# Kernel optimization log

Measured on AMD Instinct MI355X. Metric: run time of the kernel, lower is better.

## Reference

```python
import jax, jax.numpy as jnp
import numpy as np

INPUT_SIZE = 256
NUM_LABELS = 50
L = NUM_LABELS + 1  # internal label count incl. pad label (index L-1)
B, T = 64, 256


def setup_inputs() -> dict:
    key = jax.random.key(0)
    k = jax.random.split(key, 8)
    inp = {
        "input": jax.random.normal(k[0], (B, T, INPUT_SIZE), dtype=jnp.float32),
        "mask": jnp.ones((B, T), dtype=jnp.float32),
        "target": jax.random.randint(k[1], (B, T), 0, NUM_LABELS),
        # state_nn: Linear(input_size, L)
        "state_W": jax.random.normal(k[2], (INPUT_SIZE, L), dtype=jnp.float32) * 0.05,
        "state_b": jnp.zeros((L,), dtype=jnp.float32),
        # trans_nn: Linear(input_size, L*L) (bigram=True)
        "trans_W": jax.random.normal(k[3], (INPUT_SIZE, L * L), dtype=jnp.float32) * 0.05,
        "trans_b": jnp.zeros((L * L,), dtype=jnp.float32),
    }
    return inp


def _energy(x, mask, state_W, state_b, trans_W, trans_b):
    # out_s: [B,T,L]  (unary scores), out_t: [B,T,L,L] (bigram transitions)
    out_s = jnp.einsum("bti,il->btl", x, state_W) + state_b
    out_t = (jnp.einsum("bti,io->bto", x, trans_W) + trans_b).reshape(
        x.shape[0], x.shape[1], L, L
    )
    energy = out_t + out_s[:, :, None, :]  # [B,T,L,L]
    return energy * mask[:, :, None, None]


def reference(input, mask, target, state_W, state_b, trans_W, trans_b):
    """ChainCRF.loss: -log p(target | input) per batch element, shape [B]."""
    energy = _energy(input, mask, state_W, state_b, trans_W, trans_b)
    e_t = jnp.transpose(energy, (1, 0, 2, 3))  # [T,B,L,L]
    tgt_t = target.T                            # [T,B]
    msk_t = mask.T                              # [T,B]
    bidx = jnp.arange(input.shape[0])

    # t = 0: start from pad label (index L-1)
    partition0 = e_t[0][:, L - 1, :]                       # [B,L]
    tgt0 = e_t[0][bidx, L - 1, tgt_t[0]]                   # [B]

    def step(carry, xs):
        part, tgt_e, prev = carry
        curr, tgt, m = xs  # curr [B,L,L], tgt [B], m [B]
        part_new = jax.nn.logsumexp(curr + part[:, :, None], axis=1)
        part = part + (part_new - part) * m[:, None]
        tgt_e = tgt_e + curr[bidx, prev, tgt]
        return (part, tgt_e, tgt), None

    (part, tgt_e, _), _ = jax.lax.scan(
        step, (partition0, tgt0, tgt_t[0]), (e_t[1:], tgt_t[1:], msk_t[1:])
    )
    return jax.nn.logsumexp(part, axis=1) - tgt_e
```

## Files before the change

### kernel.cpp

```cpp
#include <hip/hip_runtime.h>
#include <hip/hip_bf16.h>

#define B_    64
#define T_    256
#define K_    256
#define L_    51
#define LL_   2601
#define RS_   64
#define NG_   3328
#define PST_  4096
#define MT_   128
#define NT_   128

typedef __bf16 bf16x8 __attribute__((ext_vector_type(8)));
typedef float  f32x4  __attribute__((ext_vector_type(4)));
typedef unsigned int u32x4 __attribute__((ext_vector_type(4)));
typedef u32x4 __attribute__((may_alias)) u32x4_a;
typedef unsigned long long ull;
typedef ull __attribute__((may_alias)) ull_a;
typedef unsigned short ushort_a __attribute__((may_alias));

static __device__ __forceinline__ bf16x8 as_bf16x8(u32x4 u) {
    return __builtin_bit_cast(bf16x8, u);
}
static __device__ __forceinline__ unsigned short bf16bits(float x) {
    return __builtin_bit_cast(unsigned short, __float2bfloat16(x));
}
static __device__ __forceinline__ ull pack4(f32x4 a) {
    return (ull)bf16bits(a[0]) | ((ull)bf16bits(a[1]) << 16) |
           ((ull)bf16bits(a[2]) << 32) | ((ull)bf16bits(a[3]) << 48);
}
static __device__ __forceinline__ void gld_lds16(const void* g, void* l) {
    __builtin_amdgcn_global_load_lds(
        (const __attribute__((address_space(1))) unsigned int*)g,
        (__attribute__((address_space(3))) unsigned int*)l, 16, 0, 0);
}

#define DPP_STEP(v, OP, CTRL)                                                   \
    {                                                                           \
        int _x = __builtin_bit_cast(int, v);                                    \
        float _o = __builtin_bit_cast(                                          \
            float, __builtin_amdgcn_update_dpp(_x, _x, CTRL, 0xF, 0xF, true));  \
        v = OP(v, _o);                                                          \
    }
static __device__ __forceinline__ float addf(float a, float b) { return a + b; }

__global__ __launch_bounds__(256) void prep_all(
    const float* __restrict__ trans_W, const float* __restrict__ trans_b,
    const float* __restrict__ state_W, const float* __restrict__ state_b,
    const float* __restrict__ x,
    __hip_bfloat16* __restrict__ Wt, float* __restrict__ bias,
    __hip_bfloat16* __restrict__ xb, __hip_bfloat16* __restrict__ P, int Tc)
{
    __shared__ __align__(16) __hip_bfloat16 Wl[52 * 258];
    const int blk = blockIdx.x, tid = threadIdx.x;

    if (blk < 64) {
        const int i = blk;
        if (i < L_) {
            const int jp = tid & 63, kk = tid >> 6;
            if (jp < 52) {
                for (int k = kk; k < K_; k += 4) {
                    float v = 0.f;
                    if (jp < L_) v = trans_W[(size_t)k * LL_ + i * L_ + jp] +
                                     state_W[k * L_ + jp];
                    Wl[jp * 258 + k] = __float2bfloat16(v);
                }
            }
            __syncthreads();
            for (int idx = tid; idx < 52 * 32; idx += 256) {
                const int j = idx >> 5, c = idx & 31;
                const unsigned int* row = (const unsigned int*)&Wl[j * 258];
                u32x4 v;
                v[0] = row[c * 4 + 0]; v[1] = row[c * 4 + 1];
                v[2] = row[c * 4 + 2]; v[3] = row[c * 4 + 3];
                *(u32x4*)(Wt + (size_t)((j << 6) + i) * K_ + c * 8) = v;
            }
        } else {
            const u32x4 z = {};
            for (int idx = tid; idx < 52 * 32; idx += 256) {
                const int j = idx >> 5, c = idx & 31;
                *(u32x4*)(Wt + (size_t)((j << 6) + i) * K_ + c * 8) = z;
            }
        }
        if (tid < 52) {
            const int j = tid;
            bias[(j << 6) + i] =
                (i < L_ && j < L_) ? trans_b[i * L_ + j] + state_b[j] : 0.f;
        }
    } else if (blk < 64 + 1024) {
        const int n4 = B_ * T_ * K_ / 4;
        const float4* x4 = (const float4*)x;
        ushort4* xb4 = (ushort4*)xb;
        for (int idx = (blk - 64) * 256 + tid; idx < n4; idx += 1024 * 256) {
            float4 v = x4[idx];
            ushort4 o;
            o.x = bf16bits(v.x); o.y = bf16bits(v.y);
            o.z = bf16bits(v.z); o.w = bf16bits(v.w);
            xb4[idx] = o;
        }
    } else {
        const int per = (PST_ - NG_) / 8;
        const int tot = B_ * Tc * per;
        u32x4* P16 = (u32x4*)P;
        const u32x4 z = {};
        for (int idx = (blk - 1088) * 256 + tid; idx < tot; idx += 1024 * 256) {
            const int m = idx / per;
            const int q = idx - m * per;
            P16[(size_t)m * (PST_ / 8) + (NG_ / 8) + q] = z;
        }
    }
}

__global__ __launch_bounds__(256) void gemm_energy(
    const __hip_bfloat16* __restrict__ xb,
    const __hip_bfloat16* __restrict__ Wt,
    const float* __restrict__ bias,
    const float* __restrict__ mask,
    __hip_bfloat16* __restrict__ P,
    int t0, int Tc, int TcShift)
{
    __shared__ __align__(16) __hip_bfloat16 As[MT_ * 64];
    __shared__ __align__(16) __hip_bfloat16 Bs[NT_ * 64];

    const int tid  = threadIdx.x;
    const int lane = tid & 63;
    const int wv   = tid >> 6;
    const int quad = lane >> 4;
    const int l16  = lane & 15;
    const int m0 = blockIdx.y * MT_;
    const int n0 = blockIdx.x * NT_;
    const int mrow0 = (wv >> 1) * 64;
    const int ncol0 = (wv & 1) * 64;

    f32x4 acc[4][4] = {};

    for (int kp = 0; kp < 4; ++kp) {
        if (kp) __syncthreads();
#pragma unroll
        for (int it = 0; it < 4; ++it) {
            const int s = it * 256 + tid;
            const int r = s >> 3;
            const int c = (lane & 7) ^ (r & 7);
            const int ma = m0 + r;
            const int rg = (ma >> TcShift) * T_ + t0 + (ma & (Tc - 1));
            gld_lds16((const char*)xb + (size_t)rg * 512 + kp * 128 + c * 16,
                      (char*)As + it * 4096 + wv * 1024);
            gld_lds16((const char*)Wt + (size_t)(n0 + r) * 512 + kp * 128 + c * 16,
                      (char*)Bs + it * 4096 + wv * 1024);
        }
        asm volatile("s_waitcnt vmcnt(0)" ::: "memory");
        __syncthreads();

        const u32x4_a* Av = (const u32x4_a*)As;
        const u32x4_a* Bv = (const u32x4_a*)Bs;
#pragma unroll
        for (int kk = 0; kk < 2; ++kk) {
            bf16x8 af[4], bfr[4];
#pragma unroll
            for (int f = 0; f < 4; ++f) {
                const int ra = mrow0 + f * 16 + l16;
                af[f]  = as_bf16x8(Av[ra * 8 + ((kk * 4 + quad) ^ (ra & 7))]);
                const int rb = ncol0 + f * 16 + l16;
                bfr[f] = as_bf16x8(Bv[rb * 8 + ((kk * 4 + quad) ^ (rb & 7))]);
            }
#pragma unroll
            for (int mf = 0; mf < 4; ++mf)
#pragma unroll
                for (int nf = 0; nf < 4; ++nf)
                    acc[mf][nf] = __builtin_amdgcn_mfma_f32_16x16x32_bf16(
                        af[mf], bfr[nf], acc[mf][nf], 0, 0, 0);
        }
    }
    __syncthreads();

    char* E = (char*)As;
    const int jcol = (n0 + ncol0) >> 6;
    const bool jok = jcol < L_;
    float bv[4]; bool ok[4]; int ii[4];
#pragma unroll
    for (int nf = 0; nf < 4; ++nf) {
        const int n = n0 + ncol0 + nf * 16 + l16;
        ii[nf]   = nf * 16 + l16;
        ok[nf]   = jok && (ii[nf] < L_);
        bv[nf]   = bias[n];
    }
#pragma unroll
    for (int mf = 0; mf < 4; ++mf) {
#pragma unroll
        for (int r = 0; r < 4; ++r) {
            const int ml = mrow0 + mf * 16 + quad * 4 + r;
            const int m  = m0 + ml;
            const int bb = m >> TcShift;
            const int tl = m & (Tc - 1);
            const int t  = t0 + tl;
            const float mval = mask[bb * T_ + t];
            const bool idm = (mval == 0.f) && (t != 0);
            char* erow = E + ml * 256;
            const int rot = (ml * 8) & 255;
#pragma unroll
            for (int nf = 0; nf < 4; ++nf) {
                float v;
                if (idm) v = (ok[nf] && ii[nf] == jcol) ? 1.f : 0.f;
                else     v = ok[nf] ? __expf((acc[mf][nf][r] + bv[nf]) * mval) : 0.f;
                const int nloc = ncol0 + nf * 16 + l16;
                *(ushort_a*)(erow + ((nloc * 2 + rot) & 255)) = bf16bits(v);
            }
        }
    }
    __syncthreads();

#pragma unroll
    for (int it2 = 0; it2 < 8; ++it2) {
        const int idx = it2 * 256 + tid;
        const int ml = idx >> 4, c = idx & 15;
        const char* erow = E + ml * 256;
        const int rot = (ml * 8) & 255;
        const ull lo = *(const ull_a*)(erow + ((c * 16 + rot) & 255));
        const ull hi = *(const ull_a*)(erow + ((c * 16 + 8 + rot) & 255));
        u32x4 v;
        v[0] = (unsigned int)lo; v[1] = (unsigned int)(lo >> 32);
        v[2] = (unsigned int)hi; v[3] = (unsigned int)(hi >> 32);
        *(u32x4*)(P + (size_t)(m0 + ml) * PST_ + n0 + c * 8) = v;
    }
}

__global__ __launch_bounds__(256) void prod_quad(
    const __hip_bfloat16* __restrict__ P,
    __hip_bfloat16* __restrict__ Q,
    int Tc)
{
    __shared__ u32x4 Sm[4][512];
    __shared__ __align__(16) unsigned short Tb[2][64 * 64];

    unsigned short* W2t = (unsigned short*)&Sm[0][0];
    unsigned short* W4b = (unsigned short*)&Sm[2][0];

    const int tid  = threadIdx.x;
    const int wv   = tid >> 6;
    const int lane = tid & 63;
    const int quad = lane >> 4;
    const int l16  = lane & 15;
    const int bq = blockIdx.x;
    const int Tq = Tc >> 2;
    const int b  = bq / Tq;
    const int tq = bq - b * Tq;
    const __hip_bfloat16* tile0 = P + (size_t)(b * Tc + tq * 4) * PST_;

#pragma unroll
    for (int q = 0; q < 8; ++q) {
        const int idx  = q * 4 + wv;
        const int tile = idx >> 3;
        const int part = idx & 7;
        const int slot = part * 64 + lane;
        const int r    = slot >> 3;
        const int csrc = (slot & 7) ^ (r & 7);
        gld_lds16((const char*)(tile0 + (size_t)tile * PST_) + (r * 8 + csrc) * 16,
                  (char*)&Sm[tile][part * 64]);
    }

    u32x4 idf[2];
    {
        const int e = l16 & 7;
        const unsigned int bits = (e & 1) ? 0x3F800000u : 0x3F80u;
#pragma unroll
        for (int par = 0; par < 2; ++par) {
            u32x4 v = {};
            if (quad == (l16 >> 3) + par * 2) v[e >> 1] = bits;
            idf[par] = v;
        }
    }

    auto twr = [&](unsigned short* buf, int rb, int colb, ull v) {
        *(ull_a*)((char*)buf + rb * 128 + ((colb + 16 * (rb & 7)) & 127)) = v;
    };
    auto trd = [&](const unsigned short* buf, int r, int colb) -> u32x4 {
        return *(const u32x4_a*)((char*)buf + r * 128 + ((colb + 16 * (r & 7)) & 127));
    };
    const int wcol = wv * 32 + quad * 8;

    const int ra = wv * 16 + l16;
    const f32x4 z = {};
    asm volatile("s_waitcnt vmcnt(0)" ::: "memory");
    __syncthreads();

#pragma unroll
    for (int tt = 0; tt < 2; ++tt) {
        const u32x4* S = Sm[tt * 2];
        bf16x8 a0 = as_bf16x8(S[ra * 8 + (quad ^ (ra & 7))]);
        bf16x8 a1 = as_bf16x8(S[ra * 8 + ((4 + quad) ^ (ra & 7))]);
#pragma unroll
        for (int nf = 0; nf < 4; ++nf) {
            f32x4 d = __builtin_amdgcn_mfma_f32_16x16x32_bf16(
                (nf >> 1) ? a1 : a0, as_bf16x8(idf[nf & 1]), z, 0, 0, 0);
            twr(Tb[tt], nf * 16 + l16, wcol, pack4(d));
        }
    }
    __syncthreads();

    {
        bf16x8 a2[2], a3[2];
#pragma unroll
        for (int ks = 0; ks < 2; ++ks) {
            a2[ks] = as_bf16x8(Sm[1][ra * 8 + ((ks * 4 + quad) ^ (ra & 7))]);
            a3[ks] = as_bf16x8(trd(Tb[1], ra, ks * 64 + quad * 16));
        }
        ull w2v[4], w4v[4];
#pragma unroll
        for (int nf = 0; nf < 4; ++nf) {
            const int rb = nf * 16 + l16;
            f32x4 u = z, v = z;
#pragma unroll
            for (int ks = 0; ks < 2; ++ks) {
                bf16x8 bU = as_bf16x8(trd(Tb[0], rb, ks * 64 + quad * 16));
                bf16x8 bV = as_bf16x8(Sm[3][rb * 8 + ((ks * 4 + quad) ^ (rb & 7))]);
                u = __builtin_amdgcn_mfma_f32_16x16x32_bf16(a2[ks], bU, u, 0, 0, 0);
                v = __builtin_amdgcn_mfma_f32_16x16x32_bf16(a3[ks], bV, v, 0, 0, 0);
            }
            w2v[nf] = pack4(u);
            w4v[nf] = pack4(v);
        }
        __syncthreads();
#pragma unroll
        for (int nf = 0; nf < 4; ++nf) {
            twr(W2t, nf * 16 + l16, wcol, w2v[nf]);
            twr(W4b, nf * 16 + l16, wcol, w4v[nf]);
        }
    }
    __syncthreads();

    {
        bf16x8 aw[2];
#pragma unroll
        for (int ks = 0; ks < 2; ++ks)
            aw[ks] = as_bf16x8(trd(W2t, ra, ks * 64 + quad * 16));
        ull mv[4];
#pragma unroll
        for (int nf = 0; nf < 4; ++nf) {
            const int rb = nf * 16 + l16;
            f32x4 d = z;
#pragma unroll
            for (int ks = 0; ks < 2; ++ks) {
                bf16x8 bw = as_bf16x8(trd(W4b, rb, ks * 64 + quad * 16));
                d = __builtin_amdgcn_mfma_f32_16x16x32_bf16(aw[ks], bw, d, 0, 0, 0);
            }
            mv[nf] = pack4(d);
        }
        __syncthreads();
#pragma unroll
        for (int nf = 0; nf < 4; ++nf)
            twr(Tb[0], nf * 16 + l16, wcol, mv[nf]);
    }
    __syncthreads();

    u32x4* qout = (u32x4*)(Q + (size_t)bq * PST_);
#pragma unroll
    for (int c = tid; c < 512; c += 256) {
        const int row = c >> 3;
        const int pos = c & 7;
        qout[row * 8 + pos] = trd(Tb[0], row, pos * 16);
    }
}

__global__ __launch_bounds__(128, 1) void scan_q(
    const __hip_bfloat16* __restrict__ Q,
    const __hip_bfloat16* __restrict__ P,
    const int* __restrict__ target, const float* __restrict__ mask,
    float* __restrict__ p_ws, float* __restrict__ ls_ws,
    float* __restrict__ tgt_ws, float* __restrict__ out,
    int t0q, int Tq, int Tqtot)
{
    __shared__ __align__(16) unsigned short p_arr[64];
    __shared__ float tgt_sh;

    const int b    = blockIdx.x;
    const int tid  = threadIdx.x;
    const int wv   = tid >> 6;
    const int lane = tid & 63;
    const int quad = lane >> 4;
    const int l16  = lane & 15;
    const int t0 = t0q << 2, Tc = Tq << 2;

    float pv[4] = {0.f, 0.f, 0.f, 0.f};
    float logscale = 0.f;

    if (wv == 0) {
        if (t0q == 0) {
            p_arr[lane] = (lane == L_ - 1) ? (unsigned short)0x3F80 : (unsigned short)0;
        } else {
#pragma unroll
            for (int f = 0; f < 4; ++f) pv[f] = p_ws[b * 64 + f * 16 + l16];
            logscale = ls_ws[b];
            p_arr[quad * 16 + l16] = bf16bits(pv[quad]);
        }
        asm volatile("s_waitcnt lgkmcnt(0)" ::: "memory");

        int off[8];
#pragma unroll
        for (int f = 0; f < 4; ++f)
#pragma unroll
            for (int ks = 0; ks < 2; ++ks)
                off[f * 2 + ks] = (f * 16 + l16) * 8 + ks * 4 + quad;

        const u32x4* gp = (const u32x4*)Q + (size_t)b * Tq * (PST_ / 8);
        const u32x4_a* pa = (const u32x4_a*)p_arr;

        u32x4 s0[8], s1[8], s2[8], s3[8];
        auto fetch = [&](u32x4 (&st)[8], int tl) {
            const u32x4* g = gp + (size_t)tl * (PST_ / 8);
#pragma unroll
            for (int q = 0; q < 8; ++q) st[q] = g[off[q]];
        };
        fetch(s0, 0);
        if (1 < Tq) fetch(s1, 1);
        if (2 < Tq) fetch(s2, 2);
        if (3 < Tq) fetch(s3, 3);

        auto step = [&](u32x4 (&st)[8], int tl) {
            bf16x8 a0 = as_bf16x8(pa[quad]);
            bf16x8 a1 = as_bf16x8(pa[4 + quad]);
            const f32x4 z = {};
            f32x4 ae[4], ao[4];
#pragma unroll
            for (int f = 0; f < 4; ++f) {
                ae[f] = __builtin_amdgcn_mfma_f32_16x16x32_bf16(a0, as_bf16x8(st[f * 2 + 0]), z, 0, 0, 0);
                ao[f] = __builtin_amdgcn_mfma_f32_16x16x32_bf16(a1, as_bf16x8(st[f * 2 + 1]), z, 0, 0, 0);
            }
#pragma unroll
            for (int f = 0; f < 4; ++f) pv[f] = ae[f][0] + ao[f][0];

            if (((tl & 1) == 1) || (tl == Tq - 1)) {
                float mx = fmaxf(fmaxf(pv[0], pv[1]), fmaxf(pv[2], pv[3]));
                DPP_STEP(mx, fmaxf, 0xB1);
                DPP_STEP(mx, fmaxf, 0x4E);
                DPP_STEP(mx, fmaxf, 0x124);
                DPP_STEP(mx, fmaxf, 0x128);
                const float inv = 1.f / mx;
                logscale += __logf(mx);
#pragma unroll
                for (int f = 0; f < 4; ++f) pv[f] *= inv;
            }
            p_arr[quad * 16 + l16] = bf16bits(pv[quad]);
            asm volatile("s_waitcnt lgkmcnt(0)" ::: "memory");
        };

        for (int tl = 0; tl < Tq; tl += 4) {
            step(s0, tl);
            if (tl + 4 < Tq) fetch(s0, tl + 4);
            if (tl + 1 < Tq) { step(s1, tl + 1); if (tl + 5 < Tq) fetch(s1, tl + 5); }
            if (tl + 2 < Tq) { step(s2, tl + 2); if (tl + 6 < Tq) fetch(s2, tl + 6); }
            if (tl + 3 < Tq) { step(s3, tl + 3); if (tl + 7 < Tq) fetch(s3, tl + 7); }
        }
    } else {
        float s = 0.f;
        for (int tl = lane; tl < Tc; tl += 64) {
            const int t = t0 + tl;
            const int j = target[b * T_ + t];
            const int i = (t == 0) ? (L_ - 1) : target[b * T_ + t - 1];
            const float m = (t == 0) ? 1.f : mask[b * T_ + t];
            if (m != 0.f) {
                const float pval =
                    __bfloat162float(P[(size_t)(b * Tc + tl) * PST_ + j * RS_ + i]);
                s += __logf(pval);
            }
        }
#pragma unroll
        for (int d = 1; d < 64; d <<= 1) s += __shfl_xor(s, d);
        if (lane == 0) {
            const float tot = (t0 == 0) ? s : tgt_ws[b] + s;
            tgt_ws[b] = tot;
            tgt_sh = tot;
        }
    }
    __syncthreads();

    if (wv == 0) {
        if (t0q + Tq == Tqtot) {
            float s = pv[0] + pv[1] + pv[2] + pv[3];
            DPP_STEP(s, addf, 0xB1);
            DPP_STEP(s, addf, 0x4E);
            DPP_STEP(s, addf, 0x124);
            DPP_STEP(s, addf, 0x128);
            if (lane == 0) out[b] = logscale + __logf(s) - tgt_sh;
        } else {
            if (quad == 0) {
#pragma unroll
                for (int f = 0; f < 4; ++f) p_ws[b * 64 + f * 16 + l16] = pv[f];
            }
            if (lane == 0) ls_ws[b] = logscale;
        }
    }
}

extern "C" void kernel_launch(void* const* d_in, const int* in_sizes, int n_in,
                              void* d_out, int out_size, void* d_ws, size_t ws_size,
                              hipStream_t stream)
{
    (void)in_sizes; (void)n_in; (void)out_size;
    const float* x       = (const float*)d_in[0];
    const float* mask    = (const float*)d_in[1];
    const int*   target  = (const int*)d_in[2];
    const float* state_W = (const float*)d_in[3];
    const float* state_b = (const float*)d_in[4];
    const float* trans_W = (const float*)d_in[5];
    const float* trans_b = (const float*)d_in[6];
    float* out = (float*)d_out;

    char* ws = (char*)d_ws;
    size_t off = 0;
    auto alloc = [&](size_t bytes) -> void* {
        void* p = ws + off;
        off = (off + bytes + 255) & ~(size_t)255;
        return p;
    };

    __hip_bfloat16* Wt   = (__hip_bfloat16*)alloc((size_t)NG_ * K_ * 2);
    float*          bias = (float*)alloc((size_t)NG_ * 4);
    __hip_bfloat16* xb   = (__hip_bfloat16*)alloc((size_t)B_ * T_ * K_ * 2);
    float*          p_ws = (float*)alloc((size_t)B_ * 64 * 4);
    float*          ls   = (float*)alloc((size_t)B_ * 4);
    float*          tgte = (float*)alloc((size_t)B_ * 4);
    const size_t fixed = off;

    int Tc = 256;
    while (Tc > 4 && fixed + (size_t)Tc * B_ * PST_ * 2 * 5 / 4 + 512 > ws_size) Tc >>= 1;
    __hip_bfloat16* P = (__hip_bfloat16*)alloc((size_t)Tc * B_ * PST_ * 2);
    __hip_bfloat16* Q = (__hip_bfloat16*)alloc((size_t)(Tc / 4) * B_ * PST_ * 2);
    int TcShift = 0;
    while ((1 << TcShift) < Tc) ++TcShift;

    prep_all<<<dim3(2112), 256, 0, stream>>>(
        trans_W, trans_b, state_W, state_b, x, Wt, bias, xb, P, Tc);

    for (int t0 = 0; t0 < T_; t0 += Tc) {
        gemm_energy<<<dim3(NG_ / NT_, (B_ * Tc) / MT_), 256, 0, stream>>>(
            xb, Wt, bias, mask, P, t0, Tc, TcShift);
        prod_quad<<<dim3(B_ * (Tc / 4)), 256, 0, stream>>>(P, Q, Tc);
        scan_q<<<dim3(B_), 128, 0, stream>>>(Q, P, target, mask, p_ws, ls, tgte, out,
                                             t0 / 4, Tc / 4, T_ / 4);
    }
}
```

Baseline: 209.6 us.

## Double-buffer GEMM loads, fold bias and log2e into weights, shrink P stride

The GEMM now double-buffers its K-slice loads in LDS, so global-to-LDS copies overlap the MFMA work. Bias goes into the accumulator init and log2(e) is folded into the weights, so the epilogue is a bare exp2 with a fast path when every mask value in the wave is 1. The P buffer stride shrinks from 4096 to 3328 columns, which drops the padding-zeroing pass in prep and cuts P traffic; prod_quad now zeroes the LDS padding itself. Costs are more LDS per GEMM block (about 66KB, lower occupancy) and extra code paths.

Result: faster. 197.9 us (-5.6%).

```diff
diff --git a/kernel.cpp b/kernel.cpp
--- a/kernel.cpp
+++ b/kernel.cpp
@@ -8,9 +8,11 @@
 #define LL_   2601
 #define RS_   64
 #define NG_   3328
-#define PST_  4096
+#define PSTP_ 3328
+#define PSTQ_ 4096
 #define MT_   128
 #define NT_   128
+#define LOG2E_ 1.4426950408889634f
 
 typedef __bf16 bf16x8 __attribute__((ext_vector_type(8)));
 typedef float  f32x4  __attribute__((ext_vector_type(4)));
@@ -50,7 +52,7 @@
     const float* __restrict__ state_W, const float* __restrict__ state_b,
     const float* __restrict__ x,
     __hip_bfloat16* __restrict__ Wt, float* __restrict__ bias,
-    __hip_bfloat16* __restrict__ xb, __hip_bfloat16* __restrict__ P, int Tc)
+    __hip_bfloat16* __restrict__ xb)
 {
     __shared__ __align__(16) __hip_bfloat16 Wl[52 * 258];
     const int blk = blockIdx.x, tid = threadIdx.x;
@@ -62,8 +64,8 @@
             if (jp < 52) {
                 for (int k = kk; k < K_; k += 4) {
                     float v = 0.f;
-                    if (jp < L_) v = trans_W[(size_t)k * LL_ + i * L_ + jp] +
-                                     state_W[k * L_ + jp];
+                    if (jp < L_) v = (trans_W[(size_t)k * LL_ + i * L_ + jp] +
+                                      state_W[k * L_ + jp]) * LOG2E_;
                     Wl[jp * 258 + k] = __float2bfloat16(v);
                 }
             }
@@ -86,9 +88,10 @@
         if (tid < 52) {
             const int j = tid;
             bias[(j << 6) + i] =
-                (i < L_ && j < L_) ? trans_b[i * L_ + j] + state_b[j] : 0.f;
-        }
-    } else if (blk < 64 + 1024) {
+                (i < L_ && j < L_) ? (trans_b[i * L_ + j] + state_b[j]) * LOG2E_
+                                   : 0.f;
+        }
+    } else {
         const int n4 = B_ * T_ * K_ / 4;
         const float4* x4 = (const float4*)x;
         ushort4* xb4 = (ushort4*)xb;
@@ -99,16 +102,6 @@
             o.z = bf16bits(v.z); o.w = bf16bits(v.w);
             xb4[idx] = o;
         }
-    } else {
-        const int per = (PST_ - NG_) / 8;
-        const int tot = B_ * Tc * per;
-        u32x4* P16 = (u32x4*)P;
-        const u32x4 z = {};
-        for (int idx = (blk - 1088) * 256 + tid; idx < tot; idx += 1024 * 256) {
-            const int m = idx / per;
-            const int q = idx - m * per;
-            P16[(size_t)m * (PST_ / 8) + (NG_ / 8) + q] = z;
-        }
     }
 }
 
@@ -120,8 +113,8 @@
     __hip_bfloat16* __restrict__ P,
     int t0, int Tc, int TcShift)
 {
-    __shared__ __align__(16) __hip_bfloat16 As[MT_ * 64];
-    __shared__ __align__(16) __hip_bfloat16 Bs[NT_ * 64];
+    __shared__ __align__(16) char smem[66048];
+    float* msk_sh = (float*)(smem + 65536);
 
     const int tid  = threadIdx.x;
     const int lane = tid & 63;
@@ -133,27 +126,52 @@
     const int mrow0 = (wv >> 1) * 64;
     const int ncol0 = (wv & 1) * 64;
 
-    f32x4 acc[4][4] = {};
-
+    float bv[4];
+#pragma unroll
+    for (int nf = 0; nf < 4; ++nf) bv[nf] = bias[n0 + ncol0 + nf * 16 + l16];
+
+    const char* asrc[4]; const char* bsrc[4]; char* adst[4]; char* bdst[4];
+#pragma unroll
+    for (int it = 0; it < 4; ++it) {
+        const int s = it * 256 + tid;
+        const int r = s >> 3;
+        const int c = (lane & 7) ^ (r & 7);
+        const int ma = m0 + r;
+        const int rg = (ma >> TcShift) * T_ + t0 + (ma & (Tc - 1));
+        asrc[it] = (const char*)xb + (size_t)rg * 512 + c * 16;
+        bsrc[it] = (const char*)Wt + (size_t)(n0 + r) * 512 + c * 16;
+        adst[it] = smem + it * 4096 + wv * 1024;
+        bdst[it] = smem + 32768 + it * 4096 + wv * 1024;
+    }
+    auto stage = [&](int kp, int bsel) {
+#pragma unroll
+        for (int it = 0; it < 4; ++it) {
+            gld_lds16(asrc[it] + kp * 128, adst[it] + bsel * 16384);
+            gld_lds16(bsrc[it] + kp * 128, bdst[it] + bsel * 16384);
+        }
+    };
+
+    stage(0, 0);
+
+    f32x4 acc[4][4];
+#pragma unroll
+    for (int mf = 0; mf < 4; ++mf)
+#pragma unroll
+        for (int nf = 0; nf < 4; ++nf)
+            acc[mf][nf] = (f32x4){bv[nf], bv[nf], bv[nf], bv[nf]};
+
+#pragma unroll
     for (int kp = 0; kp < 4; ++kp) {
-        if (kp) __syncthreads();
-#pragma unroll
-        for (int it = 0; it < 4; ++it) {
-            const int s = it * 256 + tid;
-            const int r = s >> 3;
-            const int c = (lane & 7) ^ (r & 7);
-            const int ma = m0 + r;
-            const int rg = (ma >> TcShift) * T_ + t0 + (ma & (Tc - 1));
-            gld_lds16((const char*)xb + (size_t)rg * 512 + kp * 128 + c * 16,
-                      (char*)As + it * 4096 + wv * 1024);
-            gld_lds16((const char*)Wt + (size_t)(n0 + r) * 512 + kp * 128 + c * 16,
-                      (char*)Bs + it * 4096 + wv * 1024);
-        }
-        asm volatile("s_waitcnt vmcnt(0)" ::: "memory");
-        __syncthreads();
-
-        const u32x4_a* Av = (const u32x4_a*)As;
-        const u32x4_a* Bv = (const u32x4_a*)Bs;
+        if (kp < 3) {
+            stage(kp + 1, (kp + 1) & 1);
+            asm volatile("s_waitcnt vmcnt(8)" ::: "memory");
+        } else {
+            asm volatile("s_waitcnt vmcnt(0)" ::: "memory");
+        }
+        __builtin_amdgcn_s_barrier();
+        const u32x4_a* Av = (const u32x4_a*)(smem + (kp & 1) * 16384);
+        const u32x4_a* Bv = (const u32x4_a*)(smem + 32768 + (kp & 1) * 16384);
+        __builtin_amdgcn_s_setprio(1);
 #pragma unroll
         for (int kk = 0; kk < 2; ++kk) {
             bf16x8 af[4], bfr[4];
@@ -171,42 +189,68 @@
                     acc[mf][nf] = __builtin_amdgcn_mfma_f32_16x16x32_bf16(
                         af[mf], bfr[nf], acc[mf][nf], 0, 0, 0);
         }
-    }
-    __syncthreads();
-
-    char* E = (char*)As;
+        __builtin_amdgcn_s_setprio(0);
+        asm volatile("s_waitcnt lgkmcnt(0)" ::: "memory");
+        __builtin_amdgcn_s_barrier();
+    }
+
+    if (tid < 128) {
+        const int m = m0 + tid;
+        msk_sh[tid] = mask[(m >> TcShift) * T_ + t0 + (m & (Tc - 1))];
+    }
+    __syncthreads();
+
+    char* E = smem;
     const int jcol = (n0 + ncol0) >> 6;
     const bool jok = jcol < L_;
-    float bv[4]; bool ok[4]; int ii[4];
-#pragma unroll
-    for (int nf = 0; nf < 4; ++nf) {
-        const int n = n0 + ncol0 + nf * 16 + l16;
-        ii[nf]   = nf * 16 + l16;
-        ok[nf]   = jok && (ii[nf] < L_);
-        bv[nf]   = bias[n];
-    }
-#pragma unroll
-    for (int mf = 0; mf < 4; ++mf) {
-#pragma unroll
-        for (int r = 0; r < 4; ++r) {
-            const int ml = mrow0 + mf * 16 + quad * 4 + r;
-            const int m  = m0 + ml;
-            const int bb = m >> TcShift;
-            const int tl = m & (Tc - 1);
-            const int t  = t0 + tl;
-            const float mval = mask[bb * T_ + t];
-            const bool idm = (mval == 0.f) && (t != 0);
-            char* erow = E + ml * 256;
-            const int rot = (ml * 8) & 255;
-#pragma unroll
-            for (int nf = 0; nf < 4; ++nf) {
-                float v;
-                if (idm) v = (ok[nf] && ii[nf] == jcol) ? 1.f : 0.f;
-                else     v = ok[nf] ? __expf((acc[mf][nf][r] + bv[nf]) * mval) : 0.f;
-                const int nloc = ncol0 + nf * 16 + l16;
-                *(ushort_a*)(erow + ((nloc * 2 + rot) & 255)) = bf16bits(v);
-            }
-        }
+    const float mlane = msk_sh[mrow0 + lane];
+    const bool fastw = __all(mlane == 1.f);
+    const int colb0 = (ncol0 + l16) * 2;
+
+    if (!jok) {
+#pragma unroll
+        for (int mf = 0; mf < 4; ++mf)
+#pragma unroll
+            for (int r = 0; r < 4; ++r) {
+                char* erow = E + (mrow0 + mf * 16 + quad * 4 + r) * 272;
+#pragma unroll
+                for (int nf = 0; nf < 4; ++nf)
+                    *(ushort_a*)(erow + colb0 + nf * 32) = 0;
+            }
+    } else if (fastw) {
+        const bool ok3 = (l16 < 3);
+#pragma unroll
+        for (int mf = 0; mf < 4; ++mf)
+#pragma unroll
+            for (int r = 0; r < 4; ++r) {
+                char* erow = E + (mrow0 + mf * 16 + quad * 4 + r) * 272;
+#pragma unroll
+                for (int nf = 0; nf < 4; ++nf) {
+                    float v = __builtin_exp2f(acc[mf][nf][r]);
+                    if (nf == 3) v = ok3 ? v : 0.f;
+                    *(ushort_a*)(erow + colb0 + nf * 32) = bf16bits(v);
+                }
+            }
+    } else {
+#pragma unroll
+        for (int mf = 0; mf < 4; ++mf)
+#pragma unroll
+            for (int r = 0; r < 4; ++r) {
+                const int ml = mrow0 + mf * 16 + quad * 4 + r;
+                const int t  = t0 + ((m0 + ml) & (Tc - 1));
+                const float mval = msk_sh[ml];
+                const bool idm = (mval == 0.f) && (t != 0);
+                char* erow = E + ml * 272;
+#pragma unroll
+                for (int nf = 0; nf < 4; ++nf) {
+                    const bool okn = (nf < 3) || (l16 < 3);
+                    const int ii = nf * 16 + l16;
+                    float v;
+                    if (idm) v = (okn && ii == jcol) ? 1.f : 0.f;
+                    else     v = okn ? __builtin_exp2f(acc[mf][nf][r] * mval) : 0.f;
+                    *(ushort_a*)(erow + colb0 + nf * 32) = bf16bits(v);
+                }
+            }
     }
     __syncthreads();
 
@@ -214,14 +258,8 @@
     for (int it2 = 0; it2 < 8; ++it2) {
         const int idx = it2 * 256 + tid;
         const int ml = idx >> 4, c = idx & 15;
-        const char* erow = E + ml * 256;
-        const int rot = (ml * 8) & 255;
-        const ull lo = *(const ull_a*)(erow + ((c * 16 + rot) & 255));
-        const ull hi = *(const ull_a*)(erow + ((c * 16 + 8 + rot) & 255));
-        u32x4 v;
-        v[0] = (unsigned int)lo; v[1] = (unsigned int)(lo >> 32);
-        v[2] = (unsigned int)hi; v[3] = (unsigned int)(hi >> 32);
-        *(u32x4*)(P + (size_t)(m0 + ml) * PST_ + n0 + c * 8) = v;
+        const u32x4 v = *(const u32x4_a*)(E + ml * 272 + c * 16);
+        *(u32x4*)(P + (size_t)(m0 + ml) * PSTP_ + n0 + c * 8) = v;
     }
 }
 
@@ -245,18 +283,25 @@
     const int Tq = Tc >> 2;
     const int b  = bq / Tq;
     const int tq = bq - b * Tq;
-    const __hip_bfloat16* tile0 = P + (size_t)(b * Tc + tq * 4) * PST_;
-
-#pragma unroll
-    for (int q = 0; q < 8; ++q) {
-        const int idx  = q * 4 + wv;
-        const int tile = idx >> 3;
-        const int part = idx & 7;
+    const __hip_bfloat16* tile0 = P + (size_t)(b * Tc + tq * 4) * PSTP_;
+
+    {
+        const u32x4 z = {};
+        for (int i2 = tid; i2 < 4 * 96; i2 += 256) {
+            const int tile = i2 / 96;
+            const int pos  = i2 - tile * 96;
+            Sm[tile][416 + pos] = z;
+        }
+    }
+#pragma unroll
+    for (int part = 0; part < 7; ++part) {
         const int slot = part * 64 + lane;
         const int r    = slot >> 3;
-        const int csrc = (slot & 7) ^ (r & 7);
-        gld_lds16((const char*)(tile0 + (size_t)tile * PST_) + (r * 8 + csrc) * 16,
-                  (char*)&Sm[tile][part * 64]);
+        if (r < 52) {
+            const int csrc = (slot & 7) ^ (r & 7);
+            gld_lds16((const char*)(tile0 + (size_t)wv * PSTP_) + (r * 8 + csrc) * 16,
+                      (char*)&Sm[wv][part * 64]);
+        }
     }
 
     u32x4 idf[2];
@@ -353,7 +398,7 @@
     }
     __syncthreads();
 
-    u32x4* qout = (u32x4*)(Q + (size_t)bq * PST_);
+    u32x4* qout = (u32x4*)(Q + (size_t)bq * PSTQ_);
 #pragma unroll
     for (int c = tid; c < 512; c += 256) {
         const int row = c >> 3;
@@ -402,12 +447,12 @@
             for (int ks = 0; ks < 2; ++ks)
                 off[f * 2 + ks] = (f * 16 + l16) * 8 + ks * 4 + quad;
 
-        const u32x4* gp = (const u32x4*)Q + (size_t)b * Tq * (PST_ / 8);
+        const u32x4* gp = (const u32x4*)Q + (size_t)b * Tq * (PSTQ_ / 8);
         const u32x4_a* pa = (const u32x4_a*)p_arr;
 
         u32x4 s0[8], s1[8], s2[8], s3[8];
         auto fetch = [&](u32x4 (&st)[8], int tl) {
-            const u32x4* g = gp + (size_t)tl * (PST_ / 8);
+            const u32x4* g = gp + (size_t)tl * (PSTQ_ / 8);
 #pragma unroll
             for (int q = 0; q < 8; ++q) st[q] = g[off[q]];
         };
@@ -460,7 +505,7 @@
             const float m = (t == 0) ? 1.f : mask[b * T_ + t];
             if (m != 0.f) {
                 const float pval =
-                    __bfloat162float(P[(size_t)(b * Tc + tl) * PST_ + j * RS_ + i]);
+                    __bfloat162float(P[(size_t)(b * Tc + tl) * PSTP_ + j * RS_ + i]);
                 s += __logf(pval);
             }
         }
@@ -523,14 +568,16 @@
     const size_t fixed = off;
 
     int Tc = 256;
-    while (Tc > 4 && fixed + (size_t)Tc * B_ * PST_ * 2 * 5 / 4 + 512 > ws_size) Tc >>= 1;
-    __hip_bfloat16* P = (__hip_bfloat16*)alloc((size_t)Tc * B_ * PST_ * 2);
-    __hip_bfloat16* Q = (__hip_bfloat16*)alloc((size_t)(Tc / 4) * B_ * PST_ * 2);
+    while (Tc > 4 && fixed + (size_t)Tc * B_ * PSTP_ * 2
+                   + (size_t)(Tc / 4) * B_ * PSTQ_ * 2 + 1024 > ws_size)
+        Tc >>= 1;
+    __hip_bfloat16* P = (__hip_bfloat16*)alloc((size_t)Tc * B_ * PSTP_ * 2);
+    __hip_bfloat16* Q = (__hip_bfloat16*)alloc((size_t)(Tc / 4) * B_ * PSTQ_ * 2);
     int TcShift = 0;
     while ((1 << TcShift) < Tc) ++TcShift;
 
-    prep_all<<<dim3(2112), 256, 0, stream>>>(
-        trans_W, trans_b, state_W, state_b, x, Wt, bias, xb, P, Tc);
+    prep_all<<<dim3(1088), 256, 0, stream>>>(
+        trans_W, trans_b, state_W, state_b, x, Wt, bias, xb);
 
     for (int t0 = 0; t0 < T_; t0 += Tc) {
         gemm_energy<<<dim3(NG_ / NT_, (B_ * Tc) / MT_), 256, 0, stream>>>(
```
